# Performance work log

Measured on AMD Instinct MI355X. Metric: run time of the kernel, lower is better.

Reference implementation:

```python
import jax, jax.numpy as jnp
import numpy as np

EPS_LN = 1e-5
EPS_BN = 1e-5


def ln_channels(x, w, b):
    # LayerNorm2d: normalize over channel dim of NCHW
    mu = x.mean(axis=1, keepdims=True)
    var = x.var(axis=1, keepdims=True)
    return (x - mu) / jnp.sqrt(var + EPS_LN) * w[None, :, None, None] + b[None, :, None, None]


def bn_eval(x, g, b):
    # eval-mode BatchNorm2d with running_mean=0, running_var=1
    return x / jnp.sqrt(1.0 + EPS_BN) * g[None, :, None, None] + b[None, :, None, None]


def conv1x1(x, w, b):
    return jnp.einsum('bchw,oc->bohw', x, w) + b[None, :, None, None]


def q_shift(x):
    # directional shift: 4 channel quarters shifted right/left/down/up by 1 px (zero pad)
    C = x.shape[1]
    q = C // 4
    return jnp.concatenate([
        jnp.pad(x[:, 0 * q:1 * q, :, :-1], ((0, 0), (0, 0), (0, 0), (1, 0))),
        jnp.pad(x[:, 1 * q:2 * q, :, 1:], ((0, 0), (0, 0), (0, 0), (0, 1))),
        jnp.pad(x[:, 2 * q:3 * q, :-1, :], ((0, 0), (0, 0), (1, 0), (0, 0))),
        jnp.pad(x[:, 3 * q:4 * q, 1:, :], ((0, 0), (0, 0), (0, 1), (0, 0))),
    ], axis=1)


def wkv_scan(k, v, w_neg, u):
    # numerically-stable RWKV WKV recurrence. k, v: [N, T, C]; w_neg (negative decay), u: [C]
    N, T, C = k.shape

    def step(carry, kv):
        a, b, p = carry
        kt, vt = kv
        q = jnp.maximum(p, u + kt)
        e1 = jnp.exp(p - q)
        e2 = jnp.exp(u + kt - q)
        out = (e1 * a + e2 * vt) / (e1 * b + e2)
        q2 = jnp.maximum(p + w_neg, kt)
        f1 = jnp.exp(p + w_neg - q2)
        f2 = jnp.exp(kt - q2)
        return (f1 * a + f2 * vt, f1 * b + f2, q2), out

    init = (jnp.zeros((N, C), k.dtype), jnp.zeros((N, C), k.dtype), jnp.full((N, C), -1e38, k.dtype))
    _, outs = jax.lax.scan(step, init, (jnp.swapaxes(k, 0, 1), jnp.swapaxes(v, 0, 1)))
    return jnp.swapaxes(outs, 0, 1)


def shape_guided_rwkv(x, mask, mix_k, mix_v, mix_r, Wk, Wv, Wr, Wo, decay, first, kn_w, kn_b):
    B, C, H, W = x.shape
    xs = q_shift(x)
    x_sh = mask * xs + (1.0 - mask) * x  # saliency-guided shift blend
    mk = mix_k[None, :, None, None]
    mv = mix_v[None, :, None, None]
    mr = mix_r[None, :, None, None]
    xk = x * mk + x_sh * (1.0 - mk)
    xv = x * mv + x_sh * (1.0 - mv)
    xr = x * mr + x_sh * (1.0 - mr)
    k = jnp.einsum('bchw,oc->bohw', xk, Wk)
    v = jnp.einsum('bchw,oc->bohw', xv, Wv)
    sr = jax.nn.sigmoid(jnp.einsum('bchw,oc->bohw', xr, Wr))
    w_neg = -jnp.exp(decay)
    # horizontal orientation: scan each row left->right
    kh = k.transpose(0, 2, 3, 1).reshape(B * H, W, C)
    vh = v.transpose(0, 2, 3, 1).reshape(B * H, W, C)
    wkv_h = wkv_scan(kh, vh, w_neg, first).reshape(B, H, W, C).transpose(0, 3, 1, 2)
    # vertical orientation: scan each column top->bottom
    kv_ = k.transpose(0, 3, 2, 1).reshape(B * W, H, C)
    vv_ = v.transpose(0, 3, 2, 1).reshape(B * W, H, C)
    wkv_v = wkv_scan(kv_, vv_, w_neg, first).reshape(B, W, H, C).transpose(0, 3, 2, 1)
    wkv = 0.5 * (wkv_h + wkv_v)
    wkv = ln_channels(wkv, kn_w, kn_b)  # key_norm=True
    out = jnp.einsum('bchw,oc->bohw', sr * wkv, Wo)
    return x + out


def channel_fusion(x, c1_w, c1_b, bn1_g, bn1_b, c2_w, c2_b, bn2_g, bn2_b, c3_w, c3_b, bn3_g, bn3_b):
    # grouped 3x3 conv (groups=2) -> GELU -> BN -> 1x1 expand -> GELU -> BN -> 1x1 reduce -> GELU -> BN
    y = jax.lax.conv_general_dilated(x, c1_w, (1, 1), 'SAME',
                                     dimension_numbers=('NCHW', 'OIHW', 'NCHW'),
                                     feature_group_count=2) + c1_b[None, :, None, None]
    y = bn_eval(jax.nn.gelu(y, approximate=False), bn1_g, bn1_b)
    y = bn_eval(jax.nn.gelu(conv1x1(y, c2_w, c2_b), approximate=False), bn2_g, bn2_b)
    y = bn_eval(jax.nn.gelu(conv1x1(y, c3_w, c3_b), approximate=False), bn3_g, bn3_b)
    return y


def patch_expand(x, up_w, up_b, s=2):
    B, C, H, W = x.shape
    y = conv1x1(x, up_w, up_b)  # [B, Cout*s*s, H, W]
    Cout = y.shape[1] // (s * s)
    y = y.reshape(B, Cout, s, s, H, W).transpose(0, 1, 4, 2, 5, 3).reshape(B, Cout, H * s, W * s)
    return y


def setup_inputs() -> dict:
    key = jax.random.key(0)
    B, C, Cs, Cout, H, W, s = 8, 256, 512, 128, 64, 64, 2
    ks = jax.random.split(key, 32)
    sc = C ** -0.5
    inp = {
        'x': jax.random.normal(ks[0], (B, C, H, W), jnp.float32),
        'skip': jax.random.normal(ks[1], (B, Cs, H, W), jnp.float32),
        'saliency_mask': jax.random.uniform(ks[2], (B, 1, H, W), jnp.float32),
        'ln1_w': jnp.ones((C,)), 'ln1_b': jnp.zeros((C,)),
        'ln2_w': jnp.ones((C,)), 'ln2_b': jnp.zeros((C,)),
        'mix_k': jax.random.uniform(ks[3], (C,)),
        'mix_v': jax.random.uniform(ks[4], (C,)),
        'mix_r': jax.random.uniform(ks[5], (C,)),
        'Wk': jax.random.normal(ks[6], (C, C)) * sc,
        'Wv': jax.random.normal(ks[7], (C, C)) * sc,
        'Wr': jax.random.normal(ks[8], (C, C)) * sc,
        'Wo': jax.random.normal(ks[9], (C, C)) * sc,
        'decay': jax.random.normal(ks[10], (C,)) * 0.5,
        'first': jax.random.normal(ks[11], (C,)) * 0.5,
        'kn_w': jnp.ones((C,)), 'kn_b': jnp.zeros((C,)),
        'sp_w': jax.random.normal(ks[12], (C, Cs)) * (Cs ** -0.5),
        'sp_b': jnp.zeros((C,)),
        'c1_w': jax.random.normal(ks[13], (2 * C, C, 3, 3)) * ((C * 9) ** -0.5),
        'c1_b': jnp.zeros((2 * C,)),
        'bn1_g': jnp.ones((2 * C,)), 'bn1_b': jnp.zeros((2 * C,)),
        'c2_w': jax.random.normal(ks[14], (4 * C, 2 * C)) * ((2 * C) ** -0.5),
        'c2_b': jnp.zeros((4 * C,)),
        'bn2_g': jnp.ones((4 * C,)), 'bn2_b': jnp.zeros((4 * C,)),
        'c3_w': jax.random.normal(ks[15], (C, 4 * C)) * ((4 * C) ** -0.5),
        'c3_b': jnp.zeros((C,)),
        'bn3_g': jnp.ones((C,)), 'bn3_b': jnp.zeros((C,)),
        'up_w': jax.random.normal(ks[16], (Cout * s * s, C)) * sc,
        'up_b': jnp.zeros((Cout * s * s,)),
    }
    return inp


def reference(x, skip, saliency_mask, ln1_w, ln1_b, ln2_w, ln2_b, mix_k, mix_v, mix_r,
              Wk, Wv, Wr, Wo, decay, first, kn_w, kn_b, sp_w, sp_b,
              c1_w, c1_b, bn1_g, bn1_b, c2_w, c2_b, bn2_g, bn2_b, c3_w, c3_b, bn3_g, bn3_b,
              up_w, up_b):
    xn = ln_channels(x, ln1_w, ln1_b)
    x_sg = shape_guided_rwkv(xn, saliency_mask, mix_k, mix_v, mix_r, Wk, Wv, Wr, Wo,
                             decay, first, kn_w, kn_b)
    skip_feat = conv1x1(skip, sp_w, sp_b)
    x_cat = jnp.concatenate([x_sg, skip_feat], axis=1)
    x_fused = channel_fusion(x_cat, c1_w, c1_b, bn1_g, bn1_b, c2_w, c2_b, bn2_g, bn2_b,
                             c3_w, c3_b, bn3_g, bn3_b)
    x_fused = ln_channels(x_fused, ln2_w, ln2_b)
    return patch_expand(x_fused, up_w, up_b, s=2)
```

## Files before the change

### kernel.cpp

```cpp
#include <hip/hip_runtime.h>
#include <hip/hip_bf16.h>
#include <math.h>

#define B_ 8
#define C_ 256
#define P_ 4096

typedef __bf16 bf16_t;
typedef __attribute__((ext_vector_type(8))) __bf16 bf16x8;
typedef __attribute__((ext_vector_type(4))) float f32x4;

template<typename T>
__global__ __launch_bounds__(256)
void ln_stats_kernel(const T* __restrict__ in, float2* __restrict__ stats)
{
    __shared__ float sred[4][64];
    __shared__ float s2red[4][64];
    int tid = threadIdx.x;
    int wp = tid & 63, cw = tid >> 6;
    int gp = blockIdx.x * 64 + wp;
    int b  = gp >> 12, p = gp & 4095;
    size_t base = (size_t)b * 256 * 4096 + p;
    float s = 0.f, s2 = 0.f;
    #pragma unroll 8
    for (int cc = 0; cc < 64; ++cc) {
        float v = (float)in[base + (size_t)(cw * 64 + cc) * 4096];
        s += v; s2 += v * v;
    }
    sred[cw][wp] = s; s2red[cw][wp] = s2;
    __syncthreads();
    if (cw == 0) {
        s  = sred[0][wp]  + sred[1][wp]  + sred[2][wp]  + sred[3][wp];
        s2 = s2red[0][wp] + s2red[1][wp] + s2red[2][wp] + s2red[3][wp];
        float mu  = s * (1.f / 256.f);
        float var = s2 * (1.f / 256.f) - mu * mu;
        stats[gp] = make_float2(mu, 1.0f / sqrtf(var + 1e-5f));
    }
}

__global__ __launch_bounds__(256)
void qshift_mix_kernel(const float* __restrict__ x, const float2* __restrict__ st1,
                       const float* __restrict__ mask,
                       const float* __restrict__ gw, const float* __restrict__ gb,
                       const float* __restrict__ mk_, const float* __restrict__ mv_,
                       const float* __restrict__ mr_,
                       bf16_t* __restrict__ xk, bf16_t* __restrict__ xv,
                       bf16_t* __restrict__ xr)
{
    int gid = blockIdx.x * 256 + threadIdx.x;
    int g = gid << 3;
    int p = g & 4095;
    int c = (g >> 12) & 255;
    int b = g >> 20;
    int h = p >> 6, w0 = p & 63;
    float gwc = gw[c], gbc = gb[c];
    int sbase = (b << 12) + p;

    float4 x0 = *reinterpret_cast<const float4*>(&x[g]);
    float4 x1 = *reinterpret_cast<const float4*>(&x[g + 4]);
    float xv8[8] = {x0.x, x0.y, x0.z, x0.w, x1.x, x1.y, x1.z, x1.w};
    float2 s8[8];
    #pragma unroll
    for (int i = 0; i < 4; ++i) {
        float4 t = *reinterpret_cast<const float4*>(&st1[sbase + i * 2]);
        s8[2 * i]     = make_float2(t.x, t.y);
        s8[2 * i + 1] = make_float2(t.z, t.w);
    }
    float xn8[8];
    #pragma unroll
    for (int i = 0; i < 8; ++i)
        xn8[i] = (xv8[i] - s8[i].x) * s8[i].y * gwc + gbc;

    float xs8[8];
    int quad = c >> 6;
    if (quad == 0) {
        xs8[0] = 0.f;
        if (w0 > 0) {
            float xm = x[g - 1]; float2 sm = st1[sbase - 1];
            xs8[0] = (xm - sm.x) * sm.y * gwc + gbc;
        }
        #pragma unroll
        for (int i = 1; i < 8; ++i) xs8[i] = xn8[i - 1];
    } else if (quad == 1) {
        #pragma unroll
        for (int i = 0; i < 7; ++i) xs8[i] = xn8[i + 1];
        xs8[7] = 0.f;
        if (w0 + 8 < 64) {
            float xp = x[g + 8]; float2 sp = st1[sbase + 8];
            xs8[7] = (xp - sp.x) * sp.y * gwc + gbc;
        }
    } else {
        int d = (quad == 2) ? -64 : 64;
        bool ok = (quad == 2) ? (h > 0) : (h < 63);
        if (ok) {
            float4 y0 = *reinterpret_cast<const float4*>(&x[g + d]);
            float4 y1 = *reinterpret_cast<const float4*>(&x[g + d + 4]);
            float yv8[8] = {y0.x, y0.y, y0.z, y0.w, y1.x, y1.y, y1.z, y1.w};
            #pragma unroll
            for (int i = 0; i < 4; ++i) {
                float4 t = *reinterpret_cast<const float4*>(&st1[sbase + d + i * 2]);
                float2 sa = make_float2(t.x, t.y), sb = make_float2(t.z, t.w);
                xs8[2 * i]     = (yv8[2 * i]     - sa.x) * sa.y * gwc + gbc;
                xs8[2 * i + 1] = (yv8[2 * i + 1] - sb.x) * sb.y * gwc + gbc;
            }
        } else {
            #pragma unroll
            for (int i = 0; i < 8; ++i) xs8[i] = 0.f;
        }
    }

    float4 m0 = *reinterpret_cast<const float4*>(&mask[sbase]);
    float4 m1 = *reinterpret_cast<const float4*>(&mask[sbase + 4]);
    float mm[8] = {m0.x, m0.y, m0.z, m0.w, m1.x, m1.y, m1.z, m1.w};
    float xsh8[8];
    #pragma unroll
    for (int i = 0; i < 8; ++i)
        xsh8[i] = mm[i] * xs8[i] + (1.f - mm[i]) * xn8[i];

    float ak = mk_[c], av = mv_[c], ar = mr_[c];
    bf16x8 ok_, ov_, or_;
    #pragma unroll
    for (int i = 0; i < 8; ++i) {
        ok_[i] = (bf16_t)(ak * xn8[i] + (1.f - ak) * xsh8[i]);
        ov_[i] = (bf16_t)(av * xn8[i] + (1.f - av) * xsh8[i]);
        or_[i] = (bf16_t)(ar * xn8[i] + (1.f - ar) * xsh8[i]);
    }
    *reinterpret_cast<bf16x8*>(&xk[g]) = ok_;
    *reinterpret_cast<bf16x8*>(&xv[g]) = ov_;
    *reinterpret_cast<bf16x8*>(&xr[g]) = or_;
}

#define EP_NONE    0
#define EP_SIGMOID 1
#define EP_BIAS    2
#define EP_RESLN   3
#define EP_GELU_BN 4
#define EP_SHUFFLE 5
#define EP_KVR     6
#define EP_WOSKIP  7

template<int NB, int BMODE, int EPI, int OUTBF, int TILE>
__global__ __launch_bounds__(256, (TILE == 64) ? 4 : 2)
void mfma_gemm(const bf16_t* __restrict__ Wp, const void* __restrict__ Xin,
               const bf16_t* __restrict__ X2,
               const float2* __restrict__ bstats, const float* __restrict__ blnw,
               const float* __restrict__ blnb,
               const float* __restrict__ bias, const float* __restrict__ skipin,
               const float* __restrict__ bng, const float* __restrict__ bnb,
               const float* __restrict__ resx, const float2* __restrict__ estats,
               const float* __restrict__ elnw, const float* __restrict__ elnb,
               void* __restrict__ OutV,
               int O, int K, int Cstride, int obs, int ocoff)
{
    constexpr int MI = TILE / 32;
    constexpr int BROWS = (NB == 3) ? 2 * 66 : TILE;
    __shared__ bf16_t Alds[NB * TILE * 36];
    __shared__ bf16_t Blds[BROWS * 36];
    int tid = threadIdx.x;
    int bx = blockIdx.x;
    int o0 = blockIdx.y * TILE;
    int b  = blockIdx.z;
    int p0 = bx * TILE;
    int cbase = (NB == 3) ? ((o0 >> 8) << 8) : 0;

    bool wo = true;
    int bb = b;
    if (EPI == EP_WOSKIP) { wo = (b >> 3) != 0; bb = b & 7; }

    const bf16_t* Wpe = Wp;
    if (EPI == EP_KVR)    Wpe = Wp + (size_t)(b >> 3) * O * K;
    if (EPI == EP_WOSKIP) Wpe = wo ? Wp : (Wp + 65536);
    int Krun = K;
    if (EPI == EP_WOSKIP) Krun = wo ? 256 : 512;

    int lane = tid & 63, wid = tid >> 6;
    int l15 = lane & 15;
    int lk8 = (lane >> 4) << 3;
    int mbase = (wid >> 1) * (TILE / 2);
    int nbase = (wid & 1) * (TILE / 2);

    const bf16_t* Xb_bf = (const bf16_t*)Xin + (size_t)bb * Cstride * 4096;
    const float*  Xb_f  = (const float*)Xin + (size_t)bb * Cstride * 4096;
    const bf16_t* X2b   = (BMODE == 3) ? X2 + (size_t)bb * Cstride * 4096 : nullptr;
    const float*  skf   = (EPI == EP_WOSKIP)
                          ? skipin + (size_t)bb * 512 * 4096 : nullptr;

    f32x4 acc[MI][MI] = {};

    if (NB == 3 && tid < 144) {
        int r = tid / 72, rest = tid % 72;
        int col = rest / 36, cc = rest % 36;
        Blds[(r * 66 + (col ? 65 : 0)) * 36 + cc] = (bf16_t)0.f;
    }

    for (int kh = 0; kh < NB; ++kh) {
        for (int c0 = 0; c0 < Krun; c0 += 32) {
            __syncthreads();
            if (NB == 3) {
                int wpos = tid & 63, cgr = tid >> 6;
                #pragma unroll
                for (int r = 0; r < 2; ++r) {
                    int hr = (bx << 1) + kh - 1 + r;
                    bf16x8 bv;
                    #pragma unroll
                    for (int i = 0; i < 8; ++i) bv[i] = (bf16_t)0.f;
                    if (hr >= 0 && hr < 64) {
                        size_t gb = (size_t)(cbase + c0 + cgr * 8) * 4096 + (hr << 6) + wpos;
                        #pragma unroll
                        for (int j = 0; j < 8; ++j) bv[j] = Xb_bf[gb + (size_t)j * 4096];
                    }
                    *reinterpret_cast<bf16x8*>(&Blds[(r * 66 + wpos + 1) * 36 + cgr * 8]) = bv;
                }
            } else {
                int p_loc = tid & (TILE - 1);
                float2 st = make_float2(0.f, 1.f);
                if (BMODE >= 2 && (EPI != EP_WOSKIP || wo))
                    st = bstats[(bb << 12) + p0 + p_loc];
                #pragma unroll
                for (int rep = 0; rep < (TILE == 128 ? 2 : 1); ++rep) {
                    int cgr = (TILE == 128) ? ((tid >> 7) + rep * 2) : (tid >> 6);
                    bf16x8 bv;
                    size_t gbase = (size_t)(c0 + cgr * 8) * 4096 + p0 + p_loc;
                    #pragma unroll
                    for (int j = 0; j < 8; ++j) {
                        size_t gi = gbase + (size_t)j * 4096;
                        int cc = c0 + cgr * 8 + j;
                        if (EPI == EP_WOSKIP && !wo) {
                            bv[j] = (bf16_t)skf[gi];
                        } else if (BMODE == 0) {
                            bv[j] = Xb_bf[gi];
                        } else if (BMODE == 1) {
                            bv[j] = (bf16_t)Xb_f[gi];
                        } else {
                            float v = ((float)Xb_bf[gi] - st.x) * st.y * blnw[cc] + blnb[cc];
                            if (BMODE == 3) v *= (float)X2b[gi];
                            bv[j] = (bf16_t)v;
                        }
                    }
                    *reinterpret_cast<bf16x8*>(&Blds[p_loc * 36 + cgr * 8]) = bv;
                }
            }
            if (TILE == 128) {
                int ao = tid >> 1, aq = tid & 1;
                #pragma unroll
                for (int t = 0; t < NB; ++t) {
                    const bf16_t* wsrc = (NB == 3)
                        ? Wpe + ((size_t)(kh * 3 + t) * O + o0 + ao) * 256 + c0
                        : Wpe + (size_t)(o0 + ao) * Krun + c0;
                    bf16x8 w0 = *reinterpret_cast<const bf16x8*>(wsrc + aq * 8);
                    bf16x8 w1 = *reinterpret_cast<const bf16x8*>(wsrc + (aq + 2) * 8);
                    *reinterpret_cast<bf16x8*>(&Alds[(t * 128 + ao) * 36 + aq * 8]) = w0;
                    *reinterpret_cast<bf16x8*>(&Alds[(t * 128 + ao) * 36 + (aq + 2) * 8]) = w1;
                }
            } else {
                int ao = tid >> 2, aq = tid & 3;
                const bf16_t* wsrc = Wpe + (size_t)(o0 + ao) * Krun + c0;
                bf16x8 w0 = *reinterpret_cast<const bf16x8*>(wsrc + aq * 8);
                *reinterpret_cast<bf16x8*>(&Alds[ao * 36 + aq * 8]) = w0;
            }
            __syncthreads();
            #pragma unroll
            for (int t = 0; t < NB; ++t) {
                bf16x8 af[MI];
                #pragma unroll
                for (int i = 0; i < MI; ++i)
                    af[i] = *reinterpret_cast<const bf16x8*>(
                              &Alds[(t * TILE + mbase + i * 16 + l15) * 36 + lk8]);
                #pragma unroll
                for (int j = 0; j < MI; ++j) {
                    int pl = nbase + j * 16;
                    int baddr;
                    if (NB == 3)
                        baddr = ((pl >> 6) * 66 + (pl & 63) + l15 + t) * 36 + lk8;
                    else
                        baddr = (pl + l15) * 36 + lk8;
                    bf16x8 bfv = *reinterpret_cast<const bf16x8*>(&Blds[baddr]);
                    #pragma unroll
                    for (int i = 0; i < MI; ++i)
                        acc[i][j] = __builtin_amdgcn_mfma_f32_16x16x32_bf16(
                                        af[i], bfv, acc[i][j], 0, 0, 0);
                }
            }
        }
    }

    const float bnsc = 1.0f / sqrtf(1.f + 1e-5f);
    bool kvr_sig = (EPI == EP_KVR) && (b >= 16);
    int oco = ocoff;
    if (EPI == EP_WOSKIP) oco = wo ? 0 : 256;
    #pragma unroll
    for (int i = 0; i < MI; ++i) {
        #pragma unroll
        for (int r = 0; r < 4; ++r) {
            int o = o0 + mbase + i * 16 + ((lane >> 4) << 2) + r;
            float bi = 0.f;
            if (EPI == EP_BIAS || EPI == EP_GELU_BN || EPI == EP_SHUFFLE) bi = bias[o];
            if (EPI == EP_WOSKIP && !wo) bi = bias[o];
            float sc = 0.f, sh = 0.f;
            if (EPI == EP_GELU_BN) { sc = bng[o] * bnsc; sh = bnb[o]; }
            float rw = 0.f, rb = 0.f;
            if ((EPI == EP_RESLN) || (EPI == EP_WOSKIP && wo)) {
                rw = elnw[o]; rb = elnb[o];
            }
            #pragma unroll
            for (int j = 0; j < MI; ++j) {
                int pp = p0 + nbase + j * 16 + l15;
                float t = acc[i][j][r];
                if (EPI == EP_SIGMOID) t = 1.f / (1.f + expf(-t));
                if (EPI == EP_KVR && kvr_sig) t = 1.f / (1.f + expf(-t));
                if (EPI == EP_BIAS || EPI == EP_GELU_BN || EPI == EP_SHUFFLE) t += bi;
                if (EPI == EP_WOSKIP && !wo) t += bi;
                if ((EPI == EP_RESLN) || (EPI == EP_WOSKIP && wo)) {
                    float2 st = estats[(bb << 12) + pp];
                    float rv = resx[((size_t)bb * 256 + o) * 4096 + pp];
                    t += (rv - st.x) * st.y * rw + rb;
                }
                if (EPI == EP_GELU_BN) {
                    t = 0.5f * t * (1.f + erff(t * 0.70710678118654752f));
                    t = t * sc + sh;
                }
                if (EPI == EP_SHUFFLE) {
                    int co = o >> 2, s1 = (o >> 1) & 1, s2 = o & 1;
                    int hh = pp >> 6, ww = pp & 63;
                    ((float*)OutV)[(((size_t)bb * 128 + co) * 128 + hh * 2 + s1) * 128
                                   + ww * 2 + s2] = t;
                } else {
                    size_t oidx = ((size_t)bb * obs + oco + o) * 4096 + pp;
                    if (OUTBF) ((bf16_t*)OutV)[oidx] = (bf16_t)t;
                    else       ((float*)OutV)[oidx]  = t;
                }
            }
        }
    }
}

__global__ __launch_bounds__(256)
void pack_all_kernel(const float* __restrict__ wk, const float* __restrict__ wv,
                     const float* __restrict__ wr, const float* __restrict__ wo,
                     const float* __restrict__ sp, const float* __restrict__ c2,
                     const float* __restrict__ c3, const float* __restrict__ up,
                     const float* __restrict__ c1, bf16_t* __restrict__ outfl,
                     bf16_t* __restrict__ outc1)
{
    int g = blockIdx.x * 256 + threadIdx.x;
    if (g < 1310720) {
        float v;
        if      (g < 65536)   v = wk[g];
        else if (g < 131072)  v = wv[g - 65536];
        else if (g < 196608)  v = wr[g - 131072];
        else if (g < 262144)  v = wo[g - 196608];
        else if (g < 393216)  v = sp[g - 262144];
        else if (g < 917504)  v = c2[g - 393216];
        else if (g < 1179648) v = c3[g - 917504];
        else                  v = up[g - 1179648];
        outfl[g] = (bf16_t)v;
    } else {
        int g2 = g - 1310720;
        if (g2 < 1179648) {
            int c = g2 & 255;
            int o = (g2 >> 8) & 511;
            int tap = g2 >> 17;
            outc1[g2] = (bf16_t)c1[(size_t)o * 2304 + c * 9 + tap];
        }
    }
}

__global__ __launch_bounds__(64)
void wkv_h_kernel(const bf16_t* __restrict__ kin, const bf16_t* __restrict__ vin,
                  bf16_t* __restrict__ outw,
                  const float* __restrict__ decay, const float* __restrict__ first)
{
    __shared__ bf16_t ks[64 * 66];
    __shared__ bf16_t vs[64 * 66];
    int c0 = blockIdx.x * 64;
    int h  = blockIdx.y;
    int b  = blockIdx.z;
    int tid = threadIdx.x;
    size_t base = (((size_t)b * 256 + c0) * 64 + h) * 64;

    for (int f = tid; f < 64 * 64; f += 64) {
        int cc = f >> 6, w = f & 63;
        ks[cc * 66 + w] = kin[base + (size_t)cc * 4096 + w];
        vs[cc * 66 + w] = vin[base + (size_t)cc * 4096 + w];
    }
    __syncthreads();

    int c = c0 + tid;
    float u  = first[c];
    float wn = -expf(decay[c]);
    float a = 0.f, bb = 0.f, pp = -1e38f;
    for (int t = 0; t < 64; ++t) {
        float kt = (float)ks[tid * 66 + t], vt = (float)vs[tid * 66 + t];
        float q  = fmaxf(pp, u + kt);
        float e1 = expf(pp - q), e2 = expf(u + kt - q);
        float ov = (e1 * a + e2 * vt) / (e1 * bb + e2);
        ks[tid * 66 + t] = (bf16_t)ov;
        float q2 = fmaxf(pp + wn, kt);
        float f1 = expf(pp + wn - q2), f2 = expf(kt - q2);
        a = f1 * a + f2 * vt;
        bb = f1 * bb + f2;
        pp = q2;
    }
    __syncthreads();
    for (int f = tid; f < 64 * 64; f += 64) {
        int cc = f >> 6, w = f & 63;
        outw[base + (size_t)cc * 4096 + w] = ks[cc * 66 + w];
    }
}

__global__ __launch_bounds__(256)
void wkv_v_kernel(const bf16_t* __restrict__ kin, const bf16_t* __restrict__ vin,
                  bf16_t* __restrict__ outw,
                  const float* __restrict__ decay, const float* __restrict__ first)
{
    int g = blockIdx.x * 256 + threadIdx.x;
    int w = g & 63;
    int c = (g >> 6) & 255;
    int b = g >> 14;
    size_t base = (size_t)(b * 256 + c) * 4096 + w;
    float u  = first[c];
    float wn = -expf(decay[c]);
    float a = 0.f, bb = 0.f, pp = -1e38f;
    for (int h = 0; h < 64; ++h) {
        size_t idx = base + h * 64;
        float kt = (float)kin[idx], vt = (float)vin[idx];
        float q  = fmaxf(pp, u + kt);
        float e1 = expf(pp - q), e2 = expf(u + kt - q);
        float ov = (e1 * a + e2 * vt) / (e1 * bb + e2);
        outw[idx] = (bf16_t)(0.5f * ((float)outw[idx] + ov));
        float q2 = fmaxf(pp + wn, kt);
        float f1 = expf(pp + wn - q2), f2 = expf(kt - q2);
        a = f1 * a + f2 * vt;
        bb = f1 * bb + f2;
        pp = q2;
    }
}

extern "C" void kernel_launch(void* const* d_in, const int* in_sizes, int n_in,
                              void* d_out, int out_size, void* d_ws, size_t ws_size,
                              hipStream_t stream)
{
    const float* x      = (const float*)d_in[0];
    const float* skip   = (const float*)d_in[1];
    const float* mask   = (const float*)d_in[2];
    const float* ln1_w  = (const float*)d_in[3];
    const float* ln1_b  = (const float*)d_in[4];
    const float* ln2_w  = (const float*)d_in[5];
    const float* ln2_b  = (const float*)d_in[6];
    const float* mix_k  = (const float*)d_in[7];
    const float* mix_v  = (const float*)d_in[8];
    const float* mix_r  = (const float*)d_in[9];
    const float* Wk     = (const float*)d_in[10];
    const float* Wv     = (const float*)d_in[11];
    const float* Wr     = (const float*)d_in[12];
    const float* Wo     = (const float*)d_in[13];
    const float* decay  = (const float*)d_in[14];
    const float* first  = (const float*)d_in[15];
    const float* kn_w   = (const float*)d_in[16];
    const float* kn_b   = (const float*)d_in[17];
    const float* sp_w   = (const float*)d_in[18];
    const float* sp_b   = (const float*)d_in[19];
    const float* c1_w   = (const float*)d_in[20];
    const float* c1_b   = (const float*)d_in[21];
    const float* bn1_g  = (const float*)d_in[22];
    const float* bn1_b  = (const float*)d_in[23];
    const float* c2_w   = (const float*)d_in[24];
    const float* c2_b   = (const float*)d_in[25];
    const float* bn2_g  = (const float*)d_in[26];
    const float* bn2_b  = (const float*)d_in[27];
    const float* c3_w   = (const float*)d_in[28];
    const float* c3_b   = (const float*)d_in[29];
    const float* bn3_g  = (const float*)d_in[30];
    const float* bn3_b  = (const float*)d_in[31];
    const float* up_w   = (const float*)d_in[32];
    const float* up_b   = (const float*)d_in[33];
    float* out = (float*)d_out;

    float* ws = (float*)d_ws;
    const size_t S = 8388608;
    const size_t Hs = S / 2;
    bf16_t* xk   = (bf16_t*)ws;
    bf16_t* xv   = (bf16_t*)(ws + Hs);
    bf16_t* xr   = (bf16_t*)(ws + 2 * Hs);
    bf16_t* kbuf = (bf16_t*)(ws + 3 * Hs);
    bf16_t* vbuf = (bf16_t*)(ws + 4 * Hs);
    bf16_t* rbuf = (bf16_t*)(ws + 5 * Hs);
    bf16_t* wkv  = (bf16_t*)(ws + 6 * Hs);
    bf16_t* xcat = (bf16_t*)(ws + 7 * Hs);
    bf16_t* y1   = (bf16_t*)(ws + 9 * Hs);
    bf16_t* y2   = (bf16_t*)ws;
    bf16_t* y3   = (bf16_t*)(ws + 4 * Hs);
    float*  wtop = ws + 11 * Hs;
    bf16_t* w9   = (bf16_t*)wtop;
    bf16_t* wfl  = w9 + 1179648;
    float2* st1  = (float2*)(wfl + 1310720);
    float2* stk  = st1 + 32768;
    float2* st2  = stk + 32768;
    bf16_t* wkb = wfl;
    bf16_t* wob = wfl + 196608;
    bf16_t* c2b = wfl + 393216;
    bf16_t* c3b = wfl + 917504;
    bf16_t* upb = wfl + 1179648;

    dim3 blk(256);

    pack_all_kernel<<<dim3(9728), blk, 0, stream>>>(Wk, Wv, Wr, Wo, sp_w, c2_w,
                                                    c3_w, up_w, c1_w, wfl, w9);
    ln_stats_kernel<float><<<dim3(512), blk, 0, stream>>>(x, st1);

    qshift_mix_kernel<<<dim3(4096), blk, 0, stream>>>(x, st1, mask, ln1_w, ln1_b,
                                                      mix_k, mix_v, mix_r, xk, xv, xr);
    mfma_gemm<1, 0, EP_KVR, 1, 64><<<dim3(64, 4, 24), blk, 0, stream>>>(
        wkb, xk, nullptr, nullptr, nullptr, nullptr, nullptr, nullptr, nullptr,
        nullptr, nullptr, nullptr, nullptr, nullptr, kbuf, 256, 256, 256, 256, 0);
    wkv_h_kernel<<<dim3(4, 64, 8), dim3(64), 0, stream>>>(kbuf, vbuf, wkv, decay, first);
    wkv_v_kernel<<<dim3(512), blk, 0, stream>>>(kbuf, vbuf, wkv, decay, first);
    ln_stats_kernel<bf16_t><<<dim3(512), blk, 0, stream>>>(wkv, stk);
    mfma_gemm<1, 3, EP_WOSKIP, 1, 64><<<dim3(64, 4, 16), blk, 0, stream>>>(
        wob, wkv, rbuf, stk, kn_w, kn_b, sp_b, skip, nullptr, nullptr,
        x, st1, ln1_w, ln1_b, xcat, 256, 0, 256, 512, 0);
    mfma_gemm<3, 0, EP_GELU_BN, 1, 128><<<dim3(32, 4, 8), blk, 0, stream>>>(
        w9, xcat, nullptr, nullptr, nullptr, nullptr, c1_b, nullptr, bn1_g, bn1_b,
        nullptr, nullptr, nullptr, nullptr, y1, 512, 256, 512, 512, 0);
    mfma_gemm<1, 0, EP_GELU_BN, 1, 128><<<dim3(32, 8, 8), blk, 0, stream>>>(
        c2b, y1, nullptr, nullptr, nullptr, nullptr, c2_b, nullptr, bn2_g, bn2_b,
        nullptr, nullptr, nullptr, nullptr, y2, 1024, 512, 512, 1024, 0);
    mfma_gemm<1, 0, EP_GELU_BN, 1, 64><<<dim3(64, 4, 8), blk, 0, stream>>>(
        c3b, y2, nullptr, nullptr, nullptr, nullptr, c3_b, nullptr, bn3_g, bn3_b,
        nullptr, nullptr, nullptr, nullptr, y3, 256, 1024, 1024, 256, 0);
    ln_stats_kernel<bf16_t><<<dim3(512), blk, 0, stream>>>(y3, st2);
    mfma_gemm<1, 2, EP_SHUFFLE, 0, 64><<<dim3(64, 8, 8), blk, 0, stream>>>(
        upb, y3, nullptr, st2, ln2_w, ln2_b, up_b, nullptr, nullptr, nullptr,
        nullptr, nullptr, nullptr, nullptr, out, 512, 256, 256, 0, 0);
}
```

Measured before the change: 479.0 us.

## Store WOSKIP output channels-last and load 3x3 conv input as vectors

The WOSKIP GEMM epilogue now stages its bf16 results in a shared-memory tile and writes them transposed to a pixel-major [B, P, 512] layout with 16-byte vector stores. The 3x3 (NB==3) conv B-tile loader reads that channels-last layout with one bf16x8 vector load per thread, replacing eight strided scalar loads. This removes uncoalesced strided gathers in the conv input path, at the cost of an extra LDS buffer and two barriers in the epilogue. The change is only correct if the NB==3 consumer is the kernel reading the WOSKIP output, because the buffer layout changes between producer and consumer.

```diff
diff --git a/kernel.cpp b/kernel.cpp
--- a/kernel.cpp
+++ b/kernel.cpp
@@ -154,8 +154,10 @@
 {
     constexpr int MI = TILE / 32;
     constexpr int BROWS = (NB == 3) ? 2 * 66 : TILE;
+    constexpr int TSZ = (EPI == EP_WOSKIP) ? 64 * 72 : 1;
     __shared__ bf16_t Alds[NB * TILE * 36];
     __shared__ bf16_t Blds[BROWS * 36];
+    __shared__ bf16_t Tlds[TSZ];
     int tid = threadIdx.x;
     int bx = blockIdx.x;
     int o0 = blockIdx.y * TILE;
@@ -197,19 +199,22 @@
         for (int c0 = 0; c0 < Krun; c0 += 32) {
             __syncthreads();
             if (NB == 3) {
-                int wpos = tid & 63, cgr = tid >> 6;
                 #pragma unroll
-                for (int r = 0; r < 2; ++r) {
-                    int hr = (bx << 1) + kh - 1 + r;
+                for (int q = 0; q < 2; ++q) {
+                    int cid = tid + q * 256;
+                    int r   = cid >> 8;
+                    int w   = (cid >> 2) & 63;
+                    int ch4 = cid & 3;
+                    int hr  = (bx << 1) + kh - 1 + r;
                     bf16x8 bv;
                     #pragma unroll
                     for (int i = 0; i < 8; ++i) bv[i] = (bf16_t)0.f;
-                    if (hr >= 0 && hr < 64) {
-                        size_t gb = (size_t)(cbase + c0 + cgr * 8) * 4096 + (hr << 6) + wpos;
-                        #pragma unroll
-                        for (int j = 0; j < 8; ++j) bv[j] = Xb_bf[gb + (size_t)j * 4096];
-                    }
-                    *reinterpret_cast<bf16x8*>(&Blds[(r * 66 + wpos + 1) * 36 + cgr * 8]) = bv;
+                    if (hr >= 0 && hr < 64)
+                        bv = *reinterpret_cast<const bf16x8*>(
+                               Xb_bf + (size_t)((hr << 6) + w) * 512
+                                     + cbase + c0 + ch4 * 8);
+                    *reinterpret_cast<bf16x8*>(
+                        &Blds[(r * 66 + w + 1) * 36 + ch4 * 8]) = bv;
                 }
             } else {
                 int p_loc = tid & (TILE - 1);
@@ -286,8 +291,44 @@
 
     const float bnsc = 1.0f / sqrtf(1.f + 1e-5f);
     bool kvr_sig = (EPI == EP_KVR) && (b >= 16);
-    int oco = ocoff;
-    if (EPI == EP_WOSKIP) oco = wo ? 0 : 256;
+
+    if (EPI == EP_WOSKIP) {
+        __syncthreads();
+        int oco = wo ? 0 : 256;
+        #pragma unroll
+        for (int i = 0; i < MI; ++i) {
+            #pragma unroll
+            for (int r = 0; r < 4; ++r) {
+                int ol = mbase + i * 16 + ((lane >> 4) << 2) + r;
+                int o = o0 + ol;
+                float bi = wo ? 0.f : bias[o];
+                float rw = 0.f, rb = 0.f;
+                if (wo) { rw = elnw[o]; rb = elnb[o]; }
+                #pragma unroll
+                for (int j = 0; j < MI; ++j) {
+                    int plc = nbase + j * 16 + l15;
+                    int pp = p0 + plc;
+                    float t = acc[i][j][r];
+                    if (!wo) t += bi;
+                    if (wo) {
+                        float2 st = estats[(bb << 12) + pp];
+                        float rv = resx[((size_t)bb * 256 + o) * 4096 + pp];
+                        t += (rv - st.x) * st.y * rw + rb;
+                    }
+                    Tlds[plc * 72 + ol] = (bf16_t)t;
+                }
+            }
+        }
+        __syncthreads();
+        int p = tid >> 2, og = tid & 3;
+        bf16x8 v0 = *reinterpret_cast<const bf16x8*>(&Tlds[p * 72 + og * 16]);
+        bf16x8 v1 = *reinterpret_cast<const bf16x8*>(&Tlds[p * 72 + og * 16 + 8]);
+        size_t orow = ((size_t)bb * 4096 + p0 + p) * 512 + oco + o0 + og * 16;
+        *reinterpret_cast<bf16x8*>(&((bf16_t*)OutV)[orow]) = v0;
+        *reinterpret_cast<bf16x8*>(&((bf16_t*)OutV)[orow + 8]) = v1;
+        return;
+    }
+
     #pragma unroll
     for (int i = 0; i < MI; ++i) {
         #pragma unroll
@@ -295,13 +336,10 @@
             int o = o0 + mbase + i * 16 + ((lane >> 4) << 2) + r;
             float bi = 0.f;
             if (EPI == EP_BIAS || EPI == EP_GELU_BN || EPI == EP_SHUFFLE) bi = bias[o];
-            if (EPI == EP_WOSKIP && !wo) bi = bias[o];
             float sc = 0.f, sh = 0.f;
             if (EPI == EP_GELU_BN) { sc = bng[o] * bnsc; sh = bnb[o]; }
             float rw = 0.f, rb = 0.f;
-            if ((EPI == EP_RESLN) || (EPI == EP_WOSKIP && wo)) {
-                rw = elnw[o]; rb = elnb[o];
-            }
+            if (EPI == EP_RESLN) { rw = elnw[o]; rb = elnb[o]; }
             #pragma unroll
             for (int j = 0; j < MI; ++j) {
                 int pp = p0 + nbase + j * 16 + l15;
@@ -309,8 +347,7 @@
                 if (EPI == EP_SIGMOID) t = 1.f / (1.f + expf(-t));
                 if (EPI == EP_KVR && kvr_sig) t = 1.f / (1.f + expf(-t));
                 if (EPI == EP_BIAS || EPI == EP_GELU_BN || EPI == EP_SHUFFLE) t += bi;
-                if (EPI == EP_WOSKIP && !wo) t += bi;
-                if ((EPI == EP_RESLN) || (EPI == EP_WOSKIP && wo)) {
+                if (EPI == EP_RESLN) {
                     float2 st = estats[(bb << 12) + pp];
                     float rv = resx[((size_t)bb * 256 + o) * 4096 + pp];
                     t += (rv - st.x) * st.y * rw + rb;
@@ -325,7 +362,7 @@
                     ((float*)OutV)[(((size_t)bb * 128 + co) * 128 + hh * 2 + s1) * 128
                                    + ww * 2 + s2] = t;
                 } else {
-                    size_t oidx = ((size_t)bb * obs + oco + o) * 4096 + pp;
+                    size_t oidx = ((size_t)bb * obs + ocoff + o) * 4096 + pp;
                     if (OUTBF) ((bf16_t*)OutV)[oidx] = (bf16_t)t;
                     else       ((float*)OutV)[oidx]  = t;
                 }
```

Measured after the change: 513.4 us. 7.2% more time.
